# Kernel tuning notes

Measured on AMD Instinct MI355X. Metric: run time of the kernel, lower is better.

Reference implementation:

```python
import jax, jax.numpy as jnp
import numpy as np

N = 50000        # node_num
E = 1600000      # num edges (avg degree 32)
IN_DIM = 128
OUT_DIM = 64
SLOPE = 0.1      # leaky relu slope_ratio
EPS = 1e-12


def setup_inputs() -> dict:
    key = jax.random.key(0)
    k0, k1, k2, k3 = jax.random.split(key, 4)
    x = jax.random.normal(k0, (N, IN_DIM), dtype=jnp.float32)
    edge_index = jax.random.randint(k1, (2, E), 0, N, dtype=jnp.int64)
    # Linear(in_dim, out_dim) params
    W = jax.random.normal(k2, (OUT_DIM, IN_DIM), dtype=jnp.float32) * (1.0 / np.sqrt(IN_DIM))
    b = jnp.zeros((OUT_DIM,), dtype=jnp.float32)
    # attention vector a: [2*out_dim, 1], kaiming-normal-ish init
    a = jax.random.normal(k3, (2 * OUT_DIM, 1), dtype=jnp.float32) * np.sqrt(2.0 / (2 * OUT_DIM))
    return {"x": x, "edge_index": edge_index, "W": W, "b": b, "a": a}


def reference(x, edge_index, W, b, a):
    # new_embeddings = Linear(x)
    new = x @ W.T + b                          # [N, OUT_DIM]
    src = edge_index[0]
    dst = edge_index[1]
    # cat(new[src], new[dst]) @ a  ==  new[src]@a_src + new[dst]@a_dst (avoids [E, 2*OUT] intermediate)
    a_src = a[:OUT_DIM, 0]                     # [OUT_DIM]
    a_dst = a[OUT_DIM:, 0]                     # [OUT_DIM]
    score = new[src] @ a_src + new[dst] @ a_dst  # [E]
    e = jnp.exp(jax.nn.leaky_relu(score, SLOPE))  # [E]
    # spmm(A, ones) -> per-row sum of edge weights; spmm(A, new) -> weighted aggregation
    row_sum = jax.ops.segment_sum(e, src, num_segments=N)                 # [N]
    results = jax.ops.segment_sum(e[:, None] * new[dst], src, num_segments=N)  # [N, OUT_DIM]
    return results / (row_sum[:, None] + EPS)
```

## Files before the change

kernel.cpp:

```cpp
#include <hip/hip_runtime.h>
#include <hip/hip_bf16.h>

#define NN    50000
#define EE    1600000
#define IND   128
#define OUTD  64
#define SLOPE 0.1f

#define BSH    5
#define BW     32
#define NB     1564
#define CAP    1408
#define CSH    8
#define NC     196
#define CAP1   8832
#define NBLK1  500
#define CHUNK1 (EE / NBLK1)
#define NLIN   (NN / 16)

typedef __attribute__((ext_vector_type(8))) short short8;
typedef __attribute__((ext_vector_type(4))) float float4v;

union SMem {
    struct {
        ushort xs[16 * 136];
        ushort wt[64 * 136];
        float  newt[16 * 68];
    } lin;
    int h[NC];
};

__global__ __launch_bounds__(256) void fused_lincoarse_kernel(
    const float* __restrict__ x, const float* __restrict__ W,
    const float* __restrict__ bias, const float* __restrict__ a,
    const int* __restrict__ ei, int* __restrict__ gcur1,
    unsigned* __restrict__ ebuf1,
    ushort* __restrict__ nbuf2, float* __restrict__ s_src, float* __restrict__ s_dst)
{
    __shared__ SMem sm;
    const int tid = threadIdx.x;

    if (blockIdx.x < NBLK1) {
        int* h = sm.h;
        for (int i = tid; i < NC; i += 256) h[i] = 0;
        __syncthreads();
        const int base = blockIdx.x * CHUNK1;
        const int4* s4p = (const int4*)(ei + base);
        for (int i = tid; i < CHUNK1 / 4; i += 256) {
            int4 s4 = s4p[i];
            atomicAdd(&h[s4.x >> CSH], 1);
            atomicAdd(&h[s4.y >> CSH], 1);
            atomicAdd(&h[s4.z >> CSH], 1);
            atomicAdd(&h[s4.w >> CSH], 1);
        }
        __syncthreads();
        for (int i = tid; i < NC; i += 256) {
            int c = h[i];
            if (c) h[i] = i * CAP1 + atomicAdd(&gcur1[i * 16], c);
        }
        __syncthreads();
        const int4* d4p = (const int4*)(ei + EE + base);
        for (int i = tid; i < CHUNK1 / 4; i += 256) {
            int4 s4 = s4p[i];
            int4 d4 = d4p[i];
            int p0 = atomicAdd(&h[s4.x >> CSH], 1);
            int p1 = atomicAdd(&h[s4.y >> CSH], 1);
            int p2 = atomicAdd(&h[s4.z >> CSH], 1);
            int p3 = atomicAdd(&h[s4.w >> CSH], 1);
            ebuf1[p0] = ((unsigned)(s4.x & 255) << 16) | (unsigned)d4.x;
            ebuf1[p1] = ((unsigned)(s4.y & 255) << 16) | (unsigned)d4.y;
            ebuf1[p2] = ((unsigned)(s4.z & 255) << 16) | (unsigned)d4.z;
            ebuf1[p3] = ((unsigned)(s4.w & 255) << 16) | (unsigned)d4.w;
        }
        return;
    }

    const int node0 = (blockIdx.x - NBLK1) * 16;
    const float4* W4 = (const float4*)W;
    #pragma unroll
    for (int i = 0; i < 8; ++i) {
        int idx = tid + i * 256;
        float4 wv = W4[idx];
        int n = idx >> 5, k = (idx & 31) * 4;
        ushort4 pk; __hip_bfloat16 h;
        h = __float2bfloat16(wv.x); pk.x = *(ushort*)&h;
        h = __float2bfloat16(wv.y); pk.y = *(ushort*)&h;
        h = __float2bfloat16(wv.z); pk.z = *(ushort*)&h;
        h = __float2bfloat16(wv.w); pk.w = *(ushort*)&h;
        *(ushort4*)&sm.lin.wt[n * 136 + k] = pk;
    }
    const float4* x4 = (const float4*)(x + (size_t)node0 * IND);
    #pragma unroll
    for (int i = 0; i < 2; ++i) {
        int idx = tid + i * 256;
        float4 xv = x4[idx];
        int r = idx >> 5, cc = (idx & 31) * 4;
        ushort4 pk; __hip_bfloat16 h;
        h = __float2bfloat16(xv.x); pk.x = *(ushort*)&h;
        h = __float2bfloat16(xv.y); pk.y = *(ushort*)&h;
        h = __float2bfloat16(xv.z); pk.z = *(ushort*)&h;
        h = __float2bfloat16(xv.w); pk.w = *(ushort*)&h;
        *(ushort4*)&sm.lin.xs[r * 136 + cc] = pk;
    }
    __syncthreads();

    const int w    = tid >> 6;
    const int lane = tid & 63;
    const int q    = lane >> 4;
    const int m16  = lane & 15;
    float4v acc = {0.f, 0.f, 0.f, 0.f};
    #pragma unroll
    for (int kk = 0; kk < IND; kk += 32) {
        short8 af = *(const short8*)&sm.lin.xs[m16 * 136 + kk + q * 8];
        short8 bf = *(const short8*)&sm.lin.wt[(w * 16 + m16) * 136 + kk + q * 8];
        acc = __builtin_amdgcn_mfma_f32_16x16x32_bf16(af, bf, acc, 0, 0, 0);
    }
    const float bv = bias[w * 16 + m16];
    #pragma unroll
    for (int r = 0; r < 4; ++r)
        sm.lin.newt[(q * 4 + r) * 68 + w * 16 + m16] = acc[r] + bv;
    __syncthreads();

    const int nl = tid >> 4;
    const int jg = tid & 15;
    const int j0 = jg * 4;
    float4 va = *(const float4*)&sm.lin.newt[nl * 68 + j0];
    const int n = node0 + nl;
    ushort4 pk;
    { __hip_bfloat16 h;
      h = __float2bfloat16(va.x); pk.x = *(ushort*)&h;
      h = __float2bfloat16(va.y); pk.y = *(ushort*)&h;
      h = __float2bfloat16(va.z); pk.z = *(ushort*)&h;
      h = __float2bfloat16(va.w); pk.w = *(ushort*)&h; }
    *(ushort4*)&nbuf2[(size_t)n * OUTD + j0] = pk;

    float ss = va.x * a[j0]        + va.y * a[j0 + 1]
             + va.z * a[j0 + 2]    + va.w * a[j0 + 3];
    float sd = va.x * a[OUTD + j0]     + va.y * a[OUTD + j0 + 1]
             + va.z * a[OUTD + j0 + 2] + va.w * a[OUTD + j0 + 3];
    #pragma unroll
    for (int m = 1; m < 16; m <<= 1) {
        ss += __shfl_xor(ss, m, 64);
        sd += __shfl_xor(sd, m, 64);
    }
    if (jg == 0) { s_src[n] = ss; s_dst[n] = sd; }
}

__global__ __launch_bounds__(256) void aggregate_kernel(
    const unsigned* __restrict__ ebuf1, const int* __restrict__ gcur1,
    const ushort* __restrict__ nbuf2,
    const float* __restrict__ s_src, const float* __restrict__ s_dst,
    float* __restrict__ out)
{
    __shared__ uint2 pairs[CAP];
    __shared__ float ssL[BW];
    __shared__ int cntL[BW], ofs[BW], cur[BW];
    const int tid  = threadIdx.x;
    const int wid  = tid >> 6;
    const int lane = tid & 63;
    const int b    = blockIdx.x;
    const int c    = b >> 3;
    const unsigned fsub = (unsigned)(b & 7);
    const int n0   = b << BSH;
    const uint2* __restrict__ nbufq = (const uint2*)nbuf2;

    if (tid < BW) {
        int n = n0 + tid;
        ssL[tid]  = (n < NN) ? s_src[n] : 0.f;
        cntL[tid] = 0;
    }
    __syncthreads();

    const int cnt1 = gcur1[c * 16];
    const unsigned* eb = ebuf1 + (size_t)c * CAP1;

    const int nv = cnt1 >> 2;
    const uint4* eb4 = (const uint4*)eb;
    for (int i = tid; i < nv; i += 256) {
        uint4 e4 = eb4[i];
        if ((e4.x >> 21) == fsub) atomicAdd(&cntL[(e4.x >> 16) & 31], 1);
        if ((e4.y >> 21) == fsub) atomicAdd(&cntL[(e4.y >> 16) & 31], 1);
        if ((e4.z >> 21) == fsub) atomicAdd(&cntL[(e4.z >> 16) & 31], 1);
        if ((e4.w >> 21) == fsub) atomicAdd(&cntL[(e4.w >> 16) & 31], 1);
    }
    for (int i = (nv << 2) + tid; i < cnt1; i += 256) {
        unsigned e = eb[i];
        if ((e >> 21) == fsub) atomicAdd(&cntL[(e >> 16) & 31], 1);
    }
    __syncthreads();

    if (wid == 0) {
        int cc = (lane < BW) ? cntL[lane] : 0;
        int sc = cc;
        #pragma unroll
        for (int m = 1; m < BW; m <<= 1) {
            int v = __shfl_up(sc, m, 64);
            if (lane >= m) sc += v;
        }
        if (lane < BW) { ofs[lane] = sc - cc; cur[lane] = sc - cc; }
    }
    __syncthreads();

    for (int i = tid; i < cnt1; i += 256) {
        unsigned e = eb[i];
        if ((e >> 21) != fsub) continue;
        int d  = e & 0xFFFFu;
        int ln = (e >> 16) & 31;
        float sc = ssL[ln] + s_dst[d];
        float lr = sc > 0.f ? sc : SLOPE * sc;
        float ev = __expf(lr);
        int pos = atomicAdd(&cur[ln], 1);
        pairs[pos] = make_uint2((unsigned)d, __float_as_uint(ev));
    }
    __syncthreads();

    const int e16 = lane >> 4;
    const int c16 = lane & 15;

    #pragma unroll 1
    for (int t = 0; t < BW / 4; ++t) {
        const int ln  = wid * (BW / 4) + t;
        const int beg = ofs[ln];
        const int len = cntL[ln];

        float a0 = 0.f, a1 = 0.f, a2 = 0.f, a3 = 0.f, es = 0.f;
        int j = 0;
        for (; j + 16 <= len; j += 16) {
            uint2 pA = pairs[beg + j + 0  + e16];
            uint2 pB = pairs[beg + j + 4  + e16];
            uint2 pC = pairs[beg + j + 8  + e16];
            uint2 pD = pairs[beg + j + 12 + e16];
            uint2 gA = nbufq[pA.x * 16 + c16];
            uint2 gB = nbufq[pB.x * 16 + c16];
            uint2 gC = nbufq[pC.x * 16 + c16];
            uint2 gD = nbufq[pD.x * 16 + c16];
            float fA = __uint_as_float(pA.y), fB = __uint_as_float(pB.y);
            float fC = __uint_as_float(pC.y), fD = __uint_as_float(pD.y);
            es += fA + fB + fC + fD;
            a0 = fmaf(fA, __uint_as_float(gA.x << 16), a0);
            a1 = fmaf(fA, __uint_as_float(gA.x & 0xFFFF0000u), a1);
            a2 = fmaf(fA, __uint_as_float(gA.y << 16), a2);
            a3 = fmaf(fA, __uint_as_float(gA.y & 0xFFFF0000u), a3);
            a0 = fmaf(fB, __uint_as_float(gB.x << 16), a0);
            a1 = fmaf(fB, __uint_as_float(gB.x & 0xFFFF0000u), a1);
            a2 = fmaf(fB, __uint_as_float(gB.y << 16), a2);
            a3 = fmaf(fB, __uint_as_float(gB.y & 0xFFFF0000u), a3);
            a0 = fmaf(fC, __uint_as_float(gC.x << 16), a0);
            a1 = fmaf(fC, __uint_as_float(gC.x & 0xFFFF0000u), a1);
            a2 = fmaf(fC, __uint_as_float(gC.y << 16), a2);
            a3 = fmaf(fC, __uint_as_float(gC.y & 0xFFFF0000u), a3);
            a0 = fmaf(fD, __uint_as_float(gD.x << 16), a0);
            a1 = fmaf(fD, __uint_as_float(gD.x & 0xFFFF0000u), a1);
            a2 = fmaf(fD, __uint_as_float(gD.y << 16), a2);
            a3 = fmaf(fD, __uint_as_float(gD.y & 0xFFFF0000u), a3);
        }
        for (; j < len; j += 4) {
            int idx = j + e16;
            uint2 p = pairs[beg + min(idx, len - 1)];
            float f = (idx < len) ? __uint_as_float(p.y) : 0.f;
            uint2 g = nbufq[p.x * 16 + c16];
            es += f;
            a0 = fmaf(f, __uint_as_float(g.x << 16), a0);
            a1 = fmaf(f, __uint_as_float(g.x & 0xFFFF0000u), a1);
            a2 = fmaf(f, __uint_as_float(g.y << 16), a2);
            a3 = fmaf(f, __uint_as_float(g.y & 0xFFFF0000u), a3);
        }
        es += __shfl_xor(es, 16, 64); es += __shfl_xor(es, 32, 64);
        a0 += __shfl_xor(a0, 16, 64); a0 += __shfl_xor(a0, 32, 64);
        a1 += __shfl_xor(a1, 16, 64); a1 += __shfl_xor(a1, 32, 64);
        a2 += __shfl_xor(a2, 16, 64); a2 += __shfl_xor(a2, 32, 64);
        a3 += __shfl_xor(a3, 16, 64); a3 += __shfl_xor(a3, 32, 64);
        const int n = n0 + ln;
        if (e16 == 0 && n < NN) {
            float inv = 1.f / (es + 1e-12f);
            float4 o = make_float4(a0 * inv, a1 * inv, a2 * inv, a3 * inv);
            *(float4*)&out[(size_t)n * OUTD + c16 * 4] = o;
        }
    }
}

extern "C" void kernel_launch(void* const* d_in, const int* in_sizes, int n_in,
                              void* d_out, int out_size, void* d_ws, size_t ws_size,
                              hipStream_t stream) {
    const float* x  = (const float*)d_in[0];
    const int*   ei = (const int*)d_in[1];
    const float* W  = (const float*)d_in[2];
    const float* b  = (const float*)d_in[3];
    const float* a  = (const float*)d_in[4];
    float* out = (float*)d_out;

    ushort*   nbuf2 = (ushort*)d_ws;
    float*    s_src = (float*)(nbuf2 + (size_t)NN * OUTD);
    float*    s_dst = s_src + NN;
    int*      gcur1 = (int*)(s_dst + NN);
    unsigned* ebuf1 = (unsigned*)(gcur1 + NC * 16);

    hipMemsetAsync(gcur1, 0, NC * 16 * sizeof(int), stream);
    fused_lincoarse_kernel<<<NBLK1 + NLIN, 256, 0, stream>>>(
        x, W, b, a, ei, gcur1, ebuf1, nbuf2, s_src, s_dst);
    aggregate_kernel<<<NB, 256, 0, stream>>>(ebuf1, gcur1, nbuf2, s_src, s_dst, out);
}
```

Baseline: 156.6 us.

## Aggregate with 128-node halves per block and stash coarse edges in registers

The aggregation kernel now launches two 512-thread blocks per coarse bucket, each covering 128 nodes, instead of eight 256-thread blocks covering 32 nodes each. This reduces how many times each bucket's edge list is read from global memory, from eight to two. Each thread keeps its edges in a register array so the second pass does not reload them. The cost is larger LDS use, a two-part scan, fewer blocks overall and higher register pressure. It also relies on an 18-entry stash and 5120-pair capacity being enough for the bucket sizes.

After: 152.8 us. 1.02x faster.

```diff
diff --git a/kernel.cpp b/kernel.cpp
--- a/kernel.cpp
+++ b/kernel.cpp
@@ -7,16 +7,15 @@
 #define OUTD  64
 #define SLOPE 0.1f
 
-#define BSH    5
-#define BW     32
-#define NB     1564
-#define CAP    1408
 #define CSH    8
 #define NC     196
 #define CAP1   8832
 #define NBLK1  500
 #define CHUNK1 (EE / NBLK1)
 #define NLIN   (NN / 16)
+#define NAGG   (NC * 2)
+#define HCAP   5120
+#define STASH  18
 
 typedef __attribute__((ext_vector_type(8))) short short8;
 typedef __attribute__((ext_vector_type(4))) float float4v;
@@ -146,25 +145,24 @@
     if (jg == 0) { s_src[n] = ss; s_dst[n] = sd; }
 }
 
-__global__ __launch_bounds__(256) void aggregate_kernel(
+__global__ __launch_bounds__(512) void aggregate_kernel(
     const unsigned* __restrict__ ebuf1, const int* __restrict__ gcur1,
     const ushort* __restrict__ nbuf2,
     const float* __restrict__ s_src, const float* __restrict__ s_dst,
     float* __restrict__ out)
 {
-    __shared__ uint2 pairs[CAP];
-    __shared__ float ssL[BW];
-    __shared__ int cntL[BW], ofs[BW], cur[BW];
+    __shared__ uint2 pairs[HCAP];
+    __shared__ float ssL[128];
+    __shared__ int cntL[128], ofs[128], cur[128];
     const int tid  = threadIdx.x;
     const int wid  = tid >> 6;
     const int lane = tid & 63;
-    const int b    = blockIdx.x;
-    const int c    = b >> 3;
-    const unsigned fsub = (unsigned)(b & 7);
-    const int n0   = b << BSH;
+    const int c    = blockIdx.x >> 1;
+    const unsigned half = blockIdx.x & 1;
+    const int n0   = (c << CSH) + ((int)half << 7);
     const uint2* __restrict__ nbufq = (const uint2*)nbuf2;
 
-    if (tid < BW) {
+    if (tid < 128) {
         int n = n0 + tid;
         ssL[tid]  = (n < NN) ? s_src[n] : 0.f;
         cntL[tid] = 0;
@@ -174,38 +172,41 @@
     const int cnt1 = gcur1[c * 16];
     const unsigned* eb = ebuf1 + (size_t)c * CAP1;
 
-    const int nv = cnt1 >> 2;
-    const uint4* eb4 = (const uint4*)eb;
-    for (int i = tid; i < nv; i += 256) {
-        uint4 e4 = eb4[i];
-        if ((e4.x >> 21) == fsub) atomicAdd(&cntL[(e4.x >> 16) & 31], 1);
-        if ((e4.y >> 21) == fsub) atomicAdd(&cntL[(e4.y >> 16) & 31], 1);
-        if ((e4.z >> 21) == fsub) atomicAdd(&cntL[(e4.z >> 16) & 31], 1);
-        if ((e4.w >> 21) == fsub) atomicAdd(&cntL[(e4.w >> 16) & 31], 1);
-    }
-    for (int i = (nv << 2) + tid; i < cnt1; i += 256) {
+    unsigned er[STASH];
+    int nk = 0;
+    for (int i = tid; i < cnt1; i += 512) {
         unsigned e = eb[i];
-        if ((e >> 21) == fsub) atomicAdd(&cntL[(e >> 16) & 31], 1);
+        er[nk++] = e;
+        if ((e >> 23) == half) atomicAdd(&cntL[(e >> 16) & 127], 1);
     }
     __syncthreads();
 
     if (wid == 0) {
-        int cc = (lane < BW) ? cntL[lane] : 0;
-        int sc = cc;
+        int c0 = cntL[lane];
+        int s0 = c0;
         #pragma unroll
-        for (int m = 1; m < BW; m <<= 1) {
-            int v = __shfl_up(sc, m, 64);
-            if (lane >= m) sc += v;
-        }
-        if (lane < BW) { ofs[lane] = sc - cc; cur[lane] = sc - cc; }
-    }
-    __syncthreads();
-
-    for (int i = tid; i < cnt1; i += 256) {
-        unsigned e = eb[i];
-        if ((e >> 21) != fsub) continue;
+        for (int m = 1; m < 64; m <<= 1) {
+            int v = __shfl_up(s0, m, 64);
+            if (lane >= m) s0 += v;
+        }
+        int tot0 = __shfl(s0, 63, 64);
+        ofs[lane] = s0 - c0; cur[lane] = s0 - c0;
+        int c1 = cntL[64 + lane];
+        int s1 = c1;
+        #pragma unroll
+        for (int m = 1; m < 64; m <<= 1) {
+            int v = __shfl_up(s1, m, 64);
+            if (lane >= m) s1 += v;
+        }
+        ofs[64 + lane] = tot0 + s1 - c1; cur[64 + lane] = tot0 + s1 - c1;
+    }
+    __syncthreads();
+
+    for (int k = 0; k < nk; ++k) {
+        unsigned e = er[k];
+        if ((e >> 23) != half) continue;
         int d  = e & 0xFFFFu;
-        int ln = (e >> 16) & 31;
+        int ln = (e >> 16) & 127;
         float sc = ssL[ln] + s_dst[d];
         float lr = sc > 0.f ? sc : SLOPE * sc;
         float ev = __expf(lr);
@@ -218,8 +219,8 @@
     const int c16 = lane & 15;
 
     #pragma unroll 1
-    for (int t = 0; t < BW / 4; ++t) {
-        const int ln  = wid * (BW / 4) + t;
+    for (int t = 0; t < 16; ++t) {
+        const int ln  = wid * 16 + t;
         const int beg = ofs[ln];
         const int len = cntL[ln];
 
@@ -298,5 +299,5 @@
     hipMemsetAsync(gcur1, 0, NC * 16 * sizeof(int), stream);
     fused_lincoarse_kernel<<<NBLK1 + NLIN, 256, 0, stream>>>(
         x, W, b, a, ei, gcur1, ebuf1, nbuf2, s_src, s_dst);
-    aggregate_kernel<<<NB, 256, 0, stream>>>(ebuf1, gcur1, nbuf2, s_src, s_dst, out);
+    aggregate_kernel<<<NAGG, 512, 0, stream>>>(ebuf1, gcur1, nbuf2, s_src, s_dst, out);
 }
```
